# Kernel tuning notes

Measured on AMD Instinct MI355X. Metric: run time of the kernel, lower is better.

The kernel has to match this reference:

```python
import jax, jax.numpy as jnp
import numpy as np

# Model dims (match init_kwargs)
B, S, D, H = 2, 1024, 1024, 8
NKV = 1024            # num_key_values = nearest square to 4*D/4 = D -> 32^2
NK = 32               # sqrt(num_key_values) = PK num_keys
NP = 2                # product_keys
DK = D // 16          # PK dim_key
TK = 8                # product_key_topk == final_topk == key_value_pk_topk


def setup_inputs() -> dict:
    key = jax.random.key(0)
    ks = jax.random.split(key, 7)
    std = jnp.float32(0.02)
    return {
        "inputs": jax.random.normal(ks[0], (B, S, D), jnp.float32),
        "Wq": jax.random.normal(ks[1], (D * H, D), jnp.float32) * std,       # to_queries (torch Linear [out,in])
        "Wpk": jax.random.normal(ks[2], (DK * NP * H, D), jnp.float32) * std, # PK.to_queries
        "pk_keys": jax.random.normal(ks[3], (NP, NK, H, DK), jnp.float32) * std,
        "keys_emb": jax.random.normal(ks[4], (NKV * H, D), jnp.float32) * std,
        "values_emb": jax.random.normal(ks[5], (NKV * H, D), jnp.float32) * std,
        "Wo": jax.random.normal(ks[6], (D, D * H), jnp.float32) * std,        # to_out
    }


def reference(inputs, Wq, Wpk, pk_keys, keys_emb, values_emb, Wo):
    b, s, d = inputs.shape
    # queries: per-head dim == d; scale by d**-0.5
    q = (inputs @ Wq.T).reshape(b, s, H, d).transpose(0, 2, 1, 3) * (d ** -0.5)  # [B,H,S,D]

    # ---- PK product-key routing ----
    pq = (inputs @ Wpk.T).reshape(b, s, NP, H, DK)
    sim = jnp.einsum('bsphd,pnhd->pbshn', pq, pk_keys)          # [NP,B,S,H,NK]
    sc, ix = jax.lax.top_k(sim, TK)                             # [NP,B,S,H,TK]
    # combine the two sub-key spaces (strides = [1, NK])
    comb_ix = (ix[0][..., :, None] + ix[1][..., None, :] * NK).reshape(b, s, H, TK * TK)
    comb_sc = (sc[0][..., :, None] + sc[1][..., None, :]).reshape(b, s, H, TK * TK)
    fsc, pki = jax.lax.top_k(comb_sc, TK)                       # final_topk = TK
    fidx = jnp.take_along_axis(comb_ix, pki, axis=-1)           # [B,S,H,TK]
    w = jax.nn.softmax(fsc, axis=-1)                            # softmax_scores=True

    # ---- per-head offset + EmbeddingBag('sum') lookups with per-sample weights ----
    idx = fidx + (jnp.arange(H) * NKV)[None, None, :, None]     # [B,S,H,TK]
    k = jnp.einsum('bshtd,bsht->bhsd', keys_emb[idx], w)        # weighted-sum bag
    v = jnp.einsum('bshtd,bsht->bhsd', values_emb[idx], w)

    # ---- causal attention ----
    att = jnp.einsum('bhqd,bhkd->bhqk', q, k)                   # [B,H,S,S]
    causal = jnp.triu(jnp.ones((s, s), bool), 1)
    att = jnp.where(causal, -jnp.finfo(att.dtype).max, att)
    att = jax.nn.softmax(att, axis=-1)
    out = jnp.einsum('bhqk,bhkd->bqhd', att, v).reshape(b, s, H * d)
    return out @ Wo.T
```

## Files before the change

### kernel.cpp

```cpp
#include <hip/hip_runtime.h>
#include <hip/hip_bf16.h>

#define BB   2
#define SS   1024
#define DD   1024
#define HH   8
#define NPP  2
#define NKK  32
#define DKK  64
#define TKK  8
#define NKV_ 1024

typedef __hip_bfloat16 bf16;
typedef __attribute__((ext_vector_type(8))) short bf16x8;
typedef __attribute__((ext_vector_type(4))) float f32x4;

using u32g = __attribute__((address_space(1))) unsigned int;
using u32l = __attribute__((address_space(3))) unsigned int;

#define GLDS16(g, l) __builtin_amdgcn_global_load_lds((const u32g*)(g), (u32l*)(l), 16, 0, 0)

__device__ inline unsigned short f2b(float f) {
    unsigned x = __float_as_uint(f);
    return (unsigned short)((x + 0x7fffu + ((x >> 16) & 1u)) >> 16);
}
__device__ inline float b2f(unsigned short u) {
    return __uint_as_float(((unsigned)u) << 16);
}

__global__ __launch_bounds__(256) void cvt_bf(const float* __restrict__ src,
                                              bf16* __restrict__ dst, long long n)
{
    long long i = ((long long)blockIdx.x * 256 + threadIdx.x) * 4;
    if (i >= n) return;
    float4 v = *(const float4*)&src[i];
    ushort4 u; u.x = f2b(v.x); u.y = f2b(v.y); u.z = f2b(v.z); u.w = f2b(v.w);
    *(ushort4*)&dst[i] = u;
}

__global__ __launch_bounds__(256) void cvt_bf3(
    const float* __restrict__ s0, bf16* __restrict__ d0, long long n0,
    const float* __restrict__ s1, bf16* __restrict__ d1, long long n1,
    const float* __restrict__ s2, bf16* __restrict__ d2, long long n2)
{
    long long i = ((long long)blockIdx.x * 256 + threadIdx.x) * 4;
    const float* s; bf16* d;
    if (i < n0)                { s = s0 + i;            d = d0 + i; }
    else if (i < n0 + n1)      { s = s1 + (i - n0);     d = d1 + (i - n0); }
    else if (i < n0 + n1 + n2) { s = s2 + (i - n0 - n1); d = d2 + (i - n0 - n1); }
    else return;
    float4 v = *(const float4*)s;
    ushort4 u; u.x = f2b(v.x); u.y = f2b(v.y); u.z = f2b(v.z); u.w = f2b(v.w);
    *(ushort4*)d = u;
}

__global__ __launch_bounds__(256) void reduce_split(
    const float* __restrict__ p, float* __restrict__ out,
    long long n, int nsplit, float scale)
{
    long long i = ((long long)blockIdx.x * 256 + threadIdx.x) * 4;
    if (i >= n) return;
    float4 a = *(const float4*)&p[i];
    for (int s = 1; s < nsplit; ++s) {
        float4 b = *(const float4*)&p[i + (long long)s * n];
        a.x += b.x; a.y += b.y; a.z += b.z; a.w += b.w;
    }
    a.x *= scale; a.y *= scale; a.z *= scale; a.w *= scale;
    *(float4*)&out[i] = a;
}

#define TILE 64
#define KT   16
#define LPAD 4

__global__ __launch_bounds__(256) void cvt3_pq(
    const float* __restrict__ s0, bf16* __restrict__ d0, long long n0,
    const float* __restrict__ s1, bf16* __restrict__ d1, long long n1,
    const float* __restrict__ s2, bf16* __restrict__ d2, long long n2,
    const float* __restrict__ A, const float* __restrict__ Bm,
    float* __restrict__ P)
{
    __shared__ float As[KT][TILE + LPAD];
    __shared__ float Bs[KT][TILE + LPAD];
    int bx = blockIdx.x;
    if (bx < 11264) {
        long long i = ((long long)bx * 256 + threadIdx.x) * 4;
        const float* s; bf16* d;
        if (i < n0)                { s = s0 + i;             d = d0 + i; }
        else if (i < n0 + n1)      { s = s1 + (i - n0);      d = d1 + (i - n0); }
        else if (i < n0 + n1 + n2) { s = s2 + (i - n0 - n1); d = d2 + (i - n0 - n1); }
        else return;
        float4 v = *(const float4*)s;
        ushort4 u; u.x = f2b(v.x); u.y = f2b(v.y); u.z = f2b(v.z); u.w = f2b(v.w);
        *(ushort4*)d = u;
        return;
    }
    int idx = bx - 11264;
    int cx = idx & 15, ky = (idx >> 4) & 3, z = idx >> 6;
    const float* Ab = A + (long long)z * 1024 * 1024;
    int col0 = cx * TILE;
    int kbase = ky * 256;
    int tid = threadIdx.x, tx = tid % 16, ty = tid / 16;
    float acc[4][4] = {{0.f}};
    int lr = tid / 4, lk = (tid % 4) * 4;

    for (int k0 = kbase; k0 < kbase + 256; k0 += KT) {
        float4 va = *(const float4*)&Ab[(long long)lr * 1024 + k0 + lk];
        As[lk + 0][lr] = va.x; As[lk + 1][lr] = va.y;
        As[lk + 2][lr] = va.z; As[lk + 3][lr] = va.w;
        float4 vb = *(const float4*)&Bm[(long long)(col0 + lr) * 1024 + k0 + lk];
        Bs[lk + 0][lr] = vb.x; Bs[lk + 1][lr] = vb.y;
        Bs[lk + 2][lr] = vb.z; Bs[lk + 3][lr] = vb.w;
        __syncthreads();
        #pragma unroll
        for (int kk = 0; kk < KT; ++kk) {
            float a[4], b[4];
            #pragma unroll
            for (int i = 0; i < 4; ++i) a[i] = As[kk][ty * 4 + i];
            #pragma unroll
            for (int j = 0; j < 4; ++j) b[j] = Bs[kk][tx * 4 + j];
            #pragma unroll
            for (int i = 0; i < 4; ++i)
                #pragma unroll
                for (int j = 0; j < 4; ++j)
                    acc[i][j] = fmaf(a[i], b[j], acc[i][j]);
        }
        __syncthreads();
    }
    long long base = ((long long)(ky * 2 + z) * 64) * 1024;
    #pragma unroll
    for (int i = 0; i < 4; ++i)
        *(float4*)&P[base + (long long)(ty * 4 + i) * 1024 + col0 + tx * 4] =
            make_float4(acc[i][0], acc[i][1], acc[i][2], acc[i][3]);
}

template<typename TC, int CAUSAL, int GROUP, int MODE>
__global__ __launch_bounds__(256) void mgemm(
    const bf16* __restrict__ A, const bf16* __restrict__ B, TC* __restrict__ C,
    int K, int lda, int ldb, int ldc,
    long long sAb, long long sAh, long long sBb, long long sBh,
    long long sCb, long long sCh, int zH, float scale,
    float* __restrict__ C2)
{
    int gx = gridDim.x, gy = gridDim.y;
    int nwg = gx * gy * gridDim.z;
    int hw  = (blockIdx.z * gy + blockIdx.y) * gx + blockIdx.x;
    int w   = (hw & 7) * (nwg >> 3) + (hw >> 3);
    int z  = w / (gx * gy);
    int r  = w % (gx * gy);
    int bx = (r / (gy * GROUP)) * GROUP + (r % GROUP);
    int by = (r / GROUP) % gy;

    int zb = z / zH, zh = z % zH;
    A += (long long)zb * sAb + (long long)zh * sAh;
    B += (long long)zb * sBb + (long long)zh * sBh;
    C += (long long)zb * sCb + (long long)zh * sCh;

    int row0 = by * 128, col0 = bx * 128;
    if (CAUSAL == 1 && col0 > row0 + 127) return;
    int Klim = (CAUSAL == 2) ? min(K, row0 + 128) : K;

    __shared__ short sh[16384];
    short* As = sh;
    short* Bs = sh + 8192;

    int tid = threadIdx.x, wave = tid >> 6, lane = tid & 63;
    int wr = wave >> 1, wc = wave & 1;
    int lr = lane & 15, lg = lane >> 4;

    f32x4 zero = {0.f, 0.f, 0.f, 0.f};
    f32x4 acc[4][4];
    #pragma unroll
    for (int m = 0; m < 4; ++m)
        #pragma unroll
        for (int n = 0; n < 4; ++n) acc[m][n] = zero;

    int srow = wave * 32 + (lane >> 3);
    int scol = ((lane & 7) ^ (lane >> 3)) * 8;
    int fo = (lg ^ (lr & 7)) * 8;

    for (int k0 = 0; k0 < Klim; k0 += 64) {
        const bf16* Ak = A + (long long)(row0 + srow) * lda + k0 + scol;
        const bf16* Bk = B + (long long)(col0 + srow) * ldb + k0 + scol;
        #pragma unroll
        for (int i = 0; i < 4; ++i) {
            GLDS16(Ak + (long long)i * 8 * lda, &As[(wave * 32 + i * 8) * 64]);
            GLDS16(Bk + (long long)i * 8 * ldb, &Bs[(wave * 32 + i * 8) * 64]);
        }
        asm volatile("s_waitcnt vmcnt(0)" ::: "memory");
        __syncthreads();

        #pragma unroll
        for (int kk = 0; kk < 2; ++kk) {
            bf16x8 af[4], bfr[4];
            #pragma unroll
            for (int m = 0; m < 4; ++m)
                af[m] = *(const bf16x8*)&As[(wr * 64 + m * 16 + lr) * 64 + (fo ^ (kk * 32))];
            #pragma unroll
            for (int n = 0; n < 4; ++n)
                bfr[n] = *(const bf16x8*)&Bs[(wc * 64 + n * 16 + lr) * 64 + (fo ^ (kk * 32))];
            #pragma unroll
            for (int m = 0; m < 4; ++m)
                #pragma unroll
                for (int n = 0; n < 4; ++n)
                    acc[m][n] = __builtin_amdgcn_mfma_f32_16x16x32_bf16(
                        bfr[n], af[m], acc[m][n], 0, 0, 0);
        }
        __syncthreads();
    }

    if constexpr (MODE == 1) {
        if (col0 >= 8192) {
            #pragma unroll
            for (int m = 0; m < 4; ++m) {
                long long row = row0 + wr * 64 + m * 16 + lr;
                #pragma unroll
                for (int n = 0; n < 4; ++n) {
                    int col = col0 - 8192 + wc * 64 + n * 16 + lg * 4;
                    *(float4*)&C2[row * 1024 + col] = make_float4(
                        acc[m][n][0], acc[m][n][1], acc[m][n][2], acc[m][n][3]);
                }
            }
            return;
        }
    }
    #pragma unroll
    for (int m = 0; m < 4; ++m) {
        long long row = row0 + wr * 64 + m * 16 + lr;
        #pragma unroll
        for (int n = 0; n < 4; ++n) {
            int col = col0 + wc * 64 + n * 16 + lg * 4;
            if constexpr (sizeof(TC) == 2) {
                ushort4 o;
                o.x = f2b(scale * acc[m][n][0]);
                o.y = f2b(scale * acc[m][n][1]);
                o.z = f2b(scale * acc[m][n][2]);
                o.w = f2b(scale * acc[m][n][3]);
                *(ushort4*)&C[row * ldc + col] = o;
            } else {
                *(float4*)&C[row * ldc + col] = make_float4(
                    scale * acc[m][n][0], scale * acc[m][n][1],
                    scale * acc[m][n][2], scale * acc[m][n][3]);
            }
        }
    }
}

__device__ inline unsigned ord_f32(float f) {
    unsigned u = __float_as_uint(f);
    return (u >> 31) ? ~u : (u | 0x80000000u);
}
__device__ inline float unord_f32(unsigned m) {
    unsigned u = (m >> 31) ? (m ^ 0x80000000u) : ~m;
    return __uint_as_float(u);
}

__global__ __launch_bounds__(256) void pk_route(
    const float* __restrict__ pq, const float* __restrict__ spl2,
    const float* __restrict__ pkk,
    float* __restrict__ wts, int* __restrict__ idxs)
{
    int bid  = blockIdx.x * 4 + (threadIdx.x >> 6);
    int lane = threadIdx.x & 63;
    int h    = bid % HH;
    long long bs = bid / HH;
    int b_ = (int)(bs >> 10), s_ = (int)(bs & 1023);
    int p = lane >> 5, n = lane & 31;

    const float* kv = pkk + ((long long)(p * NKK + n) * HH + h) * DKK;
    float s = 0.f;
    if (s_ < 64) {
        const float* q0 = spl2 + (long long)b_ * 65536
                        + (long long)s_ * 1024 + p * 512 + h * DKK;
        #pragma unroll
        for (int d = 0; d < DKK; d += 4) {
            float4 a0 = *(const float4*)&q0[d];
            float4 a1 = *(const float4*)&q0[131072 + d];
            float4 a2 = *(const float4*)&q0[262144 + d];
            float4 a3 = *(const float4*)&q0[393216 + d];
            float4 k4 = *(const float4*)&kv[d];
            float qx = ((a0.x + a1.x) + a2.x) + a3.x;
            float qy = ((a0.y + a1.y) + a2.y) + a3.y;
            float qz = ((a0.z + a1.z) + a2.z) + a3.z;
            float qw = ((a0.w + a1.w) + a2.w) + a3.w;
            s = fmaf(qx, k4.x, fmaf(qy, k4.y, fmaf(qz, k4.z, fmaf(qw, k4.w, s))));
        }
    } else {
        const float* pv = pq + (bs * NPP + p) * (HH * DKK) + h * DKK;
        #pragma unroll
        for (int d = 0; d < DKK; d += 4) {
            float4 q4 = *(const float4*)&pv[d];
            float4 k4 = *(const float4*)&kv[d];
            s = fmaf(q4.x, k4.x, fmaf(q4.y, k4.y, fmaf(q4.z, k4.z, fmaf(q4.w, k4.w, s))));
        }
    }

    unsigned long long key =
        ((unsigned long long)ord_f32(s) << 32) | (unsigned)(31 - n);
    #pragma unroll
    for (int k = 2; k <= 32; k <<= 1) {
        #pragma unroll
        for (int j = k >> 1; j > 0; j >>= 1) {
            unsigned long long other = __shfl_xor(key, j);
            bool keep_big = ((n & k) == 0) == ((n & j) == 0);
            key = (keep_big == (other > key)) ? other : key;
        }
    }
    float keepv = unord_f32((unsigned)(key >> 32));
    int   keepn = 31 - (int)(key & 31);

    int l5 = lane & 31;
    int ii, jj;
    if (l5 < 8)       { ii = 0;       jj = l5; }
    else if (l5 < 12) { ii = 1;       jj = l5 - 8; }
    else if (l5 < 14) { ii = 2;       jj = l5 - 12; }
    else if (l5 < 16) { ii = 3;       jj = l5 - 14; }
    else              { ii = l5 - 12; jj = 0; }
    float c0 = __shfl(keepv, ii);
    float c1 = __shfl(keepv, 32 + jj);
    float cv = c0 + c1;
    int fcell = ii * 8 + jj;

    unsigned long long k2 = (l5 < 20)
        ? (((unsigned long long)ord_f32(cv) << 32) | (unsigned)(63 - fcell))
        : 0ull;
    #pragma unroll
    for (int k = 2; k <= 32; k <<= 1) {
        #pragma unroll
        for (int j = k >> 1; j > 0; j >>= 1) {
            unsigned long long other = __shfl_xor(k2, j);
            bool keep_big = ((l5 & k) == 0) == ((l5 & j) == 0);
            k2 = (keep_big == (other > k2)) ? other : k2;
        }
    }
    int   f   = 63 - (int)(k2 & 63);
    float fsv = unord_f32((unsigned)(k2 >> 32));
    int n0 = __shfl(keepn, f >> 3);
    int n1 = __shfl(keepn, 32 + (f & 7));
    int fsi = n0 + n1 * NKK;

    float m0 = __shfl(fsv, 0);
    float e = (lane < TKK) ? expf(fsv - m0) : 0.f;
    float sum = e;
    #pragma unroll
    for (int off = 1; off < 8; off <<= 1) sum += __shfl_xor(sum, off);
    if (lane < TKK) {
        wts[(long long)bid * TKK + lane]  = e / sum;
        idxs[(long long)bid * TKK + lane] = fsi + h * NKV_;
    }
}

__global__ __launch_bounds__(256) void gather_kv(
    const bf16* __restrict__ keb, const bf16* __restrict__ veb,
    const float* __restrict__ wts, const int* __restrict__ idxs,
    bf16* __restrict__ kb, bf16* __restrict__ vsd)
{
    int bid = blockIdx.x;
    int h = bid % HH;
    int bs = bid / HH;
    int b = bs / SS, s = bs % SS;

    float w[TKK]; long long rb[TKK];
    #pragma unroll
    for (int t = 0; t < TKK; ++t) {
        w[t]  = wts[(long long)bid * TKK + t];
        rb[t] = (long long)idxs[(long long)bid * TKK + t] * DD;
    }
    int c0 = threadIdx.x * 4;
    long long off = (((long long)b * HH + h) * SS + s) * DD + c0;

    ushort4 ld[TKK];
    #pragma unroll
    for (int t = 0; t < TKK; ++t) ld[t] = *(const ushort4*)&keb[rb[t] + c0];
    float4 a = {0.f, 0.f, 0.f, 0.f};
    #pragma unroll
    for (int t = 0; t < TKK; ++t) {
        a.x += w[t] * b2f(ld[t].x); a.y += w[t] * b2f(ld[t].y);
        a.z += w[t] * b2f(ld[t].z); a.w += w[t] * b2f(ld[t].w);
    }
    ushort4 o; o.x = f2b(a.x); o.y = f2b(a.y); o.z = f2b(a.z); o.w = f2b(a.w);
    *(ushort4*)&kb[off] = o;

    #pragma unroll
    for (int t = 0; t < TKK; ++t) ld[t] = *(const ushort4*)&veb[rb[t] + c0];
    a = make_float4(0.f, 0.f, 0.f, 0.f);
    #pragma unroll
    for (int t = 0; t < TKK; ++t) {
        a.x += w[t] * b2f(ld[t].x); a.y += w[t] * b2f(ld[t].y);
        a.z += w[t] * b2f(ld[t].z); a.w += w[t] * b2f(ld[t].w);
    }
    o.x = f2b(a.x); o.y = f2b(a.y); o.z = f2b(a.z); o.w = f2b(a.w);
    *(ushort4*)&vsd[off] = o;
}

__global__ __launch_bounds__(256) void softmax_tr(
    bf16* __restrict__ sc, bf16* __restrict__ vtm)
{
    __shared__ unsigned short La[64][65];
    __shared__ unsigned short Lb[64][65];
    int bx = blockIdx.x;

    if (bx < 4096) {
        int r    = bx * 4 + (threadIdx.x >> 6);
        int lane = threadIdx.x & 63;
        int sq   = r % SS;
        unsigned short* row = (unsigned short*)(sc + (long long)r * SS);
        int nvalid = sq + 1;
        int wlim = ((sq >> 7) + 1) << 7;
        int base = lane * 16;

        uint4 u0 = *(const uint4*)&row[base];
        uint4 u1 = *(const uint4*)&row[base + 8];
        unsigned uw[8] = {u0.x, u0.y, u0.z, u0.w, u1.x, u1.y, u1.z, u1.w};

        float v[16];
        float m = -INFINITY;
        #pragma unroll
        for (int i = 0; i < 8; ++i) {
            int j0 = base + i * 2;
            v[i*2]   = (j0     < nvalid) ? __uint_as_float(uw[i] << 16)          : -INFINITY;
            v[i*2+1] = (j0 + 1 < nvalid) ? __uint_as_float(uw[i] & 0xffff0000u) : -INFINITY;
            m = fmaxf(m, fmaxf(v[i*2], v[i*2+1]));
        }
        #pragma unroll
        for (int off = 1; off < 64; off <<= 1) m = fmaxf(m, __shfl_xor(m, off));

        float e[16], ls = 0.f;
        #pragma unroll
        for (int i = 0; i < 16; ++i) {
            e[i] = (base + i < nvalid) ? expf(v[i] - m) : 0.f;
            ls += e[i];
        }
        #pragma unroll
        for (int off = 1; off < 64; off <<= 1) ls += __shfl_xor(ls, off);
        float inv = 1.f / ls;

        if (base < wlim) {
            unsigned ow[8];
            #pragma unroll
            for (int i = 0; i < 8; ++i)
                ow[i] = (unsigned)f2b(e[i*2] * inv) | ((unsigned)f2b(e[i*2+1] * inv) << 16);
            *(uint4*)&row[base]     = make_uint4(ow[0], ow[1], ow[2], ow[3]);
            *(uint4*)&row[base + 8] = make_uint4(ow[4], ow[5], ow[6], ow[7]);
        }
        return;
    }

    int idx = bx - 4096;
    int p = idx % 136;
    long long zz = idx / 136;
    unsigned short* M = (unsigned short*)vtm + zz * SS * DD;

    int ti = 0;
    while (p >= 16 - ti) { p -= 16 - ti; ++ti; }
    int tj = ti + p;
    int a0r = ti * 64, a0c = tj * 64;
    int b0r = tj * 64, b0c = ti * 64;

    int r = threadIdx.x / 16, c4 = (threadIdx.x % 16) * 4;
    #pragma unroll
    for (int i = 0; i < 4; ++i) {
        int sr = r + i * 16;
        ushort4 va = *(const ushort4*)&M[(long long)(a0r + sr) * DD + a0c + c4];
        La[sr][c4] = va.x; La[sr][c4+1] = va.y; La[sr][c4+2] = va.z; La[sr][c4+3] = va.w;
        if (ti != tj) {
            ushort4 vb = *(const ushort4*)&M[(long long)(b0r + sr) * DD + b0c + c4];
            Lb[sr][c4] = vb.x; Lb[sr][c4+1] = vb.y; Lb[sr][c4+2] = vb.z; Lb[sr][c4+3] = vb.w;
        }
    }
    __syncthreads();
    #pragma unroll
    for (int i = 0; i < 4; ++i) {
        int dr = r + i * 16;
        ushort4 va;
        va.x = La[c4][dr]; va.y = La[c4+1][dr]; va.z = La[c4+2][dr]; va.w = La[c4+3][dr];
        *(ushort4*)&M[(long long)(b0r + dr) * DD + b0c + c4] = va;
        if (ti != tj) {
            ushort4 vb;
            vb.x = Lb[c4][dr]; vb.y = Lb[c4+1][dr]; vb.z = Lb[c4+2][dr]; vb.w = Lb[c4+3][dr];
            *(ushort4*)&M[(long long)(a0r + dr) * DD + a0c + c4] = vb;
        }
    }
}

extern "C" void kernel_launch(void* const* d_in, const int* in_sizes, int n_in,
                              void* d_out, int out_size, void* d_ws, size_t ws_size,
                              hipStream_t stream)
{
    const float* inputs     = (const float*)d_in[0];
    const float* Wq         = (const float*)d_in[1];
    const float* Wpk        = (const float*)d_in[2];
    const float* pk_keys    = (const float*)d_in[3];
    const float* keys_emb   = (const float*)d_in[4];
    const float* values_emb = (const float*)d_in[5];
    const float* Wo         = (const float*)d_in[6];
    float* out = (float*)d_out;

    const long long MB = 1LL << 20;
    char* base = (char*)d_ws;
    bf16* kb  = (bf16*)(base);
    float* spl = (float*)base;
    float* spl2 = (float*)(base + 16*MB);
    bf16* qc  = (bf16*)(base + 32*MB);
    bf16* vt  = (bf16*)(base + 64*MB);
    char* screg = base + 96*MB;
    bf16* scb = (bf16*)screg;
    float* pqb = (float*)screg;
    bf16* Wqb  = (bf16*)(screg + 8*MB);
    bf16* Wpkb = (bf16*)(screg + 24*MB);
    bf16* xb   = (bf16*)(screg + 26*MB);
    bf16* keb  = (bf16*)screg;
    bf16* veb  = (bf16*)(screg + 16*MB);
    bf16* Wob  = (bf16*)screg;
    float* wtb = (float*)(base + 128*MB);
    int*   ixb = (int*)(base + 128*MB + (512<<10));
    size_t needed = (size_t)(129*MB);
    if (ws_size < needed) return;

    const long long SLAB = (long long)SS * HH * DD;
    const long long SD   = (long long)SS * DD;
    const long long OUTN = 2048LL * 1024;

    cvt3_pq<<<dim3(11392), 256, 0, stream>>>(
        inputs, xb, 2097152LL, Wq, Wqb, 8388608LL, Wpk, Wpkb, 1048576LL,
        inputs, Wpk, spl2);

    mgemm<bf16, 0, 8, 1><<<dim3(72, 16, 1), 256, 0, stream>>>(
        xb, Wqb, qc, 1024, 1024, 1024, 8192,
        0, 0, 0, 0, 0, 0, 1, 0.03125f, pqb);

    pk_route<<<dim3(BB * SS * HH / 4), 256, 0, stream>>>(
        pqb, spl2, pk_keys, wtb, ixb);

    cvt_bf3<<<dim3(16384), 256, 0, stream>>>(
        keys_emb, keb, 8388608LL, values_emb, veb, 8388608LL,
        (const float*)nullptr, (bf16*)nullptr, 0LL);

    gather_kv<<<dim3(BB * SS * HH), 256, 0, stream>>>(
        keb, veb, wtb, ixb, kb, vt);

    mgemm<bf16, 1, 1, 0><<<dim3(8, 8, BB * HH), 256, 0, stream>>>(
        qc, kb, scb, 1024, 8192, 1024, 1024,
        SLAB, (long long)DD, (long long)HH * SD, SD,
        (long long)HH * SS * SS, (long long)SS * SS, HH, 1.0f, nullptr);

    softmax_tr<<<dim3(4096 + 2176), 256, 0, stream>>>(scb, vt);

    mgemm<bf16, 2, 1, 0><<<dim3(8, 8, BB * HH), 256, 0, stream>>>(
        scb, vt, qc, 1024, 1024, 1024, 8192,
        (long long)HH * SS * SS, (long long)SS * SS,
        (long long)HH * SD, SD,
        SLAB, (long long)DD, HH, 1.0f, nullptr);

    cvt_bf<<<dim3(8192), 256, 0, stream>>>(Wo, Wob, 8388608LL);

    mgemm<float, 0, 1, 0><<<dim3(8, 16, 4), 256, 0, stream>>>(
        qc, Wob, spl, 2048, 8192, 8192, 1024,
        2048, 0, 2048, 0, OUTN, 0, 1, 1.0f, nullptr);
    reduce_split<<<dim3(2048), 256, 0, stream>>>(spl, out, OUTN, 4, 1.0f);
}
```

Baseline: 348.7 us.

## Fuse bf16 conversions into routing and softmax kernels, deepen output split-K

The keys/values embedding conversion now runs as extra blocks in the PK routing kernel, and the Wo conversion runs as extra blocks in the softmax/transpose kernel, which removes two standalone launches. The workspace layout is reshuffled so Wob, pqb and the split-K partials no longer alias live buffers. The final output GEMM splits K into 8 chunks of 1024 instead of 4 chunks of 2048, giving more blocks, and reduce_split sums 8 partials. The cost is extra partial-buffer traffic and a larger reduction.

After: 347.8 us. Within noise of the previous version (-0.2%).

```diff
diff --git a/kernel.cpp b/kernel.cpp
--- a/kernel.cpp
+++ b/kernel.cpp
@@ -27,28 +27,7 @@
 __device__ inline float b2f(unsigned short u) {
     return __uint_as_float(((unsigned)u) << 16);
 }
-
-__global__ __launch_bounds__(256) void cvt_bf(const float* __restrict__ src,
-                                              bf16* __restrict__ dst, long long n)
-{
-    long long i = ((long long)blockIdx.x * 256 + threadIdx.x) * 4;
-    if (i >= n) return;
-    float4 v = *(const float4*)&src[i];
-    ushort4 u; u.x = f2b(v.x); u.y = f2b(v.y); u.z = f2b(v.z); u.w = f2b(v.w);
-    *(ushort4*)&dst[i] = u;
-}
-
-__global__ __launch_bounds__(256) void cvt_bf3(
-    const float* __restrict__ s0, bf16* __restrict__ d0, long long n0,
-    const float* __restrict__ s1, bf16* __restrict__ d1, long long n1,
-    const float* __restrict__ s2, bf16* __restrict__ d2, long long n2)
-{
-    long long i = ((long long)blockIdx.x * 256 + threadIdx.x) * 4;
-    const float* s; bf16* d;
-    if (i < n0)                { s = s0 + i;            d = d0 + i; }
-    else if (i < n0 + n1)      { s = s1 + (i - n0);     d = d1 + (i - n0); }
-    else if (i < n0 + n1 + n2) { s = s2 + (i - n0 - n1); d = d2 + (i - n0 - n1); }
-    else return;
+__device__ inline void cvt4(const float* s, bf16* d) {
     float4 v = *(const float4*)s;
     ushort4 u; u.x = f2b(v.x); u.y = f2b(v.y); u.z = f2b(v.z); u.w = f2b(v.w);
     *(ushort4*)d = u;
@@ -85,14 +64,9 @@
     int bx = blockIdx.x;
     if (bx < 11264) {
         long long i = ((long long)bx * 256 + threadIdx.x) * 4;
-        const float* s; bf16* d;
-        if (i < n0)                { s = s0 + i;             d = d0 + i; }
-        else if (i < n0 + n1)      { s = s1 + (i - n0);      d = d1 + (i - n0); }
-        else if (i < n0 + n1 + n2) { s = s2 + (i - n0 - n1); d = d2 + (i - n0 - n1); }
-        else return;
-        float4 v = *(const float4*)s;
-        ushort4 u; u.x = f2b(v.x); u.y = f2b(v.y); u.z = f2b(v.z); u.w = f2b(v.w);
-        *(ushort4*)d = u;
+        if (i < n0)                cvt4(s0 + i,             d0 + i);
+        else if (i < n0 + n1)      cvt4(s1 + (i - n0),      d1 + (i - n0));
+        else if (i < n0 + n1 + n2) cvt4(s2 + (i - n0 - n1), d2 + (i - n0 - n1));
         return;
     }
     int idx = bx - 11264;
@@ -255,12 +229,22 @@
     return __uint_as_float(u);
 }
 
-__global__ __launch_bounds__(256) void pk_route(
+__global__ __launch_bounds__(256) void route_cvt(
     const float* __restrict__ pq, const float* __restrict__ spl2,
     const float* __restrict__ pkk,
-    float* __restrict__ wts, int* __restrict__ idxs)
-{
-    int bid  = blockIdx.x * 4 + (threadIdx.x >> 6);
+    float* __restrict__ wts, int* __restrict__ idxs,
+    const float* __restrict__ ke, bf16* __restrict__ keb,
+    const float* __restrict__ ve, bf16* __restrict__ veb)
+{
+    int bxx = blockIdx.x;
+    if (bxx >= 4096) {
+        long long i = ((long long)(bxx - 4096) * 256 + threadIdx.x) * 4;
+        if (i < 8388608LL) cvt4(ke + i, keb + i);
+        else               cvt4(ve + (i - 8388608LL), veb + (i - 8388608LL));
+        return;
+    }
+
+    int bid  = bxx * 4 + (threadIdx.x >> 6);
     int lane = threadIdx.x & 63;
     int h    = bid % HH;
     long long bs = bid / HH;
@@ -393,13 +377,19 @@
     *(ushort4*)&vsd[off] = o;
 }
 
-__global__ __launch_bounds__(256) void softmax_tr(
-    bf16* __restrict__ sc, bf16* __restrict__ vtm)
+__global__ __launch_bounds__(256) void softmax_tr_cvt(
+    bf16* __restrict__ sc, bf16* __restrict__ vtm,
+    const float* __restrict__ Wo, bf16* __restrict__ Wob)
 {
     __shared__ unsigned short La[64][65];
     __shared__ unsigned short Lb[64][65];
     int bx = blockIdx.x;
 
+    if (bx >= 6272) {
+        long long i = ((long long)(bx - 6272) * 256 + threadIdx.x) * 4;
+        cvt4(Wo + i, Wob + i);
+        return;
+    }
     if (bx < 4096) {
         int r    = bx * 4 + (threadIdx.x >> 6);
         int lane = threadIdx.x & 63;
@@ -498,20 +488,20 @@
 
     const long long MB = 1LL << 20;
     char* base = (char*)d_ws;
-    bf16* kb  = (bf16*)(base);
-    float* spl = (float*)base;
+    bf16* kb   = (bf16*)(base);
+    bf16* Wob  = (bf16*)(base);
     float* spl2 = (float*)(base + 16*MB);
+    float* pqb  = (float*)(base + 18*MB);
     bf16* qc  = (bf16*)(base + 32*MB);
     bf16* vt  = (bf16*)(base + 64*MB);
+    float* spl = (float*)(base + 64*MB);
     char* screg = base + 96*MB;
     bf16* scb = (bf16*)screg;
-    float* pqb = (float*)screg;
     bf16* Wqb  = (bf16*)(screg + 8*MB);
     bf16* Wpkb = (bf16*)(screg + 24*MB);
     bf16* xb   = (bf16*)(screg + 26*MB);
     bf16* keb  = (bf16*)screg;
     bf16* veb  = (bf16*)(screg + 16*MB);
-    bf16* Wob  = (bf16*)screg;
     float* wtb = (float*)(base + 128*MB);
     int*   ixb = (int*)(base + 128*MB + (512<<10));
     size_t needed = (size_t)(129*MB);
@@ -529,12 +519,8 @@
         xb, Wqb, qc, 1024, 1024, 1024, 8192,
         0, 0, 0, 0, 0, 0, 1, 0.03125f, pqb);
 
-    pk_route<<<dim3(BB * SS * HH / 4), 256, 0, stream>>>(
-        pqb, spl2, pk_keys, wtb, ixb);
-
-    cvt_bf3<<<dim3(16384), 256, 0, stream>>>(
-        keys_emb, keb, 8388608LL, values_emb, veb, 8388608LL,
-        (const float*)nullptr, (bf16*)nullptr, 0LL);
+    route_cvt<<<dim3(4096 + 16384), 256, 0, stream>>>(
+        pqb, spl2, pk_keys, wtb, ixb, keys_emb, keb, values_emb, veb);
 
     gather_kv<<<dim3(BB * SS * HH), 256, 0, stream>>>(
         keb, veb, wtb, ixb, kb, vt);
@@ -544,7 +530,8 @@
         SLAB, (long long)DD, (long long)HH * SD, SD,
         (long long)HH * SS * SS, (long long)SS * SS, HH, 1.0f, nullptr);
 
-    softmax_tr<<<dim3(4096 + 2176), 256, 0, stream>>>(scb, vt);
+    softmax_tr_cvt<<<dim3(4096 + 2176 + 8192), 256, 0, stream>>>(
+        scb, vt, Wo, Wob);
 
     mgemm<bf16, 2, 1, 0><<<dim3(8, 8, BB * HH), 256, 0, stream>>>(
         scb, vt, qc, 1024, 1024, 1024, 8192,
@@ -552,10 +539,8 @@
         (long long)HH * SD, SD,
         SLAB, (long long)DD, HH, 1.0f, nullptr);
 
-    cvt_bf<<<dim3(8192), 256, 0, stream>>>(Wo, Wob, 8388608LL);
-
-    mgemm<float, 0, 1, 0><<<dim3(8, 16, 4), 256, 0, stream>>>(
-        qc, Wob, spl, 2048, 8192, 8192, 1024,
-        2048, 0, 2048, 0, OUTN, 0, 1, 1.0f, nullptr);
-    reduce_split<<<dim3(2048), 256, 0, stream>>>(spl, out, OUTN, 4, 1.0f);
-}
+    mgemm<float, 0, 1, 0><<<dim3(8, 16, 8), 256, 0, stream>>>(
+        qc, Wob, spl, 1024, 8192, 8192, 1024,
+        1024, 0, 1024, 0, OUTN, 0, 1, 1.0f, nullptr);
+    reduce_split<<<dim3(2048), 256, 0, stream>>>(spl, out, OUTN, 8, 1.0f);
+}
```
